# Kernel tuning notes

Hardware: AMD Instinct MI355X
Metric: run time of the kernel (lower is better)

Reference implementation:

```python
import jax, jax.numpy as jnp
import numpy as np

V = 4          # view_num
B = 2048       # batch_size
D = 512        # feature dim
N = V * B
TEMP = 0.5     # temperature
EPS = 1e-8     # torch CosineSimilarity eps


def _neg_idx():
    # Row with residue p (position within its view block) masks out columns c
    # with c % B == p (the positive/self positions), exactly matching
    # mask_positive_samples: fill_diagonal_(0) on every BxB block.
    cols = np.arange(N)
    return np.stack([cols[cols % B != p] for p in range(B)])  # [B, N-V]

_NEG_IDX = jnp.asarray(_neg_idx())


def setup_inputs() -> dict:
    key = jax.random.key(0)
    x = jax.random.normal(key, (V, B, D), dtype=jnp.float32)
    return {"x": x}


def reference(x):
    # torch.cat(input, dim=0) -> [N, D]
    xf = x.reshape(N, D)
    # Cosine similarity via normalize + matmul (same math as broadcasted
    # CosineSimilarity(dim=2), expressed efficiently).
    norm = jnp.maximum(jnp.linalg.norm(xf, axis=1, keepdims=True), EPS)
    xn = xf / norm
    sim = (xn @ xn.T) / TEMP                                  # [N, N]

    # Negatives per anchor row: gather masked columns (same column order as
    # torch boolean-mask indexing, which is row-major ascending).
    sim_v = sim.reshape(V, B, N)
    negs = jnp.take_along_axis(sim_v, _NEG_IDX[None], axis=2)  # [V, B, N-V]
    lse_neg = jax.nn.logsumexp(negs, axis=2)                   # [V, B]

    # pos[i, j, b] = sim block-diagonal between views i and j
    pos = jnp.diagonal(sim.reshape(V, B, V, B), axis1=1, axis2=3)  # [V, V, B]

    # CrossEntropy with label 0 on logits = [pos_ij, negatives_i]:
    #   loss_b = logsumexp([pos, negs]) - pos = logaddexp(pos, lse_neg) - pos
    lse = jnp.logaddexp(pos, lse_neg[:, None, :])              # [V, V, B]
    per_pair = (lse - pos).sum(axis=2) / B                     # [V, V]

    off_diag = 1.0 - jnp.eye(V, dtype=per_pair.dtype)          # skip j == i
    return jnp.sum(per_pair * off_diag)
```

## Files before the change

kernel.cpp:

```cpp
#include <hip/hip_runtime.h>
#include <hip/hip_fp8.h>

#define NV 4
#define NB 2048
#define ND 512
#define NN 8192

typedef int int8v __attribute__((ext_vector_type(8)));
typedef int int4v __attribute__((ext_vector_type(4)));
typedef float floatx4 __attribute__((ext_vector_type(4)));
#define SCALE1 0x7F7F7F7Fu

__global__ __launch_bounds__(256) void normalize_k(const float* __restrict__ x,
                                                   unsigned char* __restrict__ xn,
                                                   float* __restrict__ sumexp,
                                                   float* __restrict__ out) {
  if (threadIdx.x < 4) sumexp[blockIdx.x * 4 + threadIdx.x] = 0.0f;
  if (blockIdx.x == 0 && threadIdx.x == 0) out[0] = 0.0f;

  const int row = blockIdx.x * 4 + (threadIdx.x >> 6);
  const int l = threadIdx.x & 63;
  const float4* xr = (const float4*)(x + (size_t)row * ND);
  float4 v0 = xr[l * 2 + 0];
  float4 v1 = xr[l * 2 + 1];
  float ss = v0.x * v0.x + v0.y * v0.y + v0.z * v0.z + v0.w * v0.w +
             v1.x * v1.x + v1.y * v1.y + v1.z * v1.z + v1.w * v1.w;
#pragma unroll
  for (int off = 32; off > 0; off >>= 1) ss += __shfl_xor(ss, off, 64);
  const float inv = 1.0f / fmaxf(sqrtf(ss), 1e-8f);
  union { unsigned char b[8]; uint2 u; } pk;
  pk.b[0] = __hip_fp8_e4m3(v0.x * inv).__x;
  pk.b[1] = __hip_fp8_e4m3(v0.y * inv).__x;
  pk.b[2] = __hip_fp8_e4m3(v0.z * inv).__x;
  pk.b[3] = __hip_fp8_e4m3(v0.w * inv).__x;
  pk.b[4] = __hip_fp8_e4m3(v1.x * inv).__x;
  pk.b[5] = __hip_fp8_e4m3(v1.y * inv).__x;
  pk.b[6] = __hip_fp8_e4m3(v1.z * inv).__x;
  pk.b[7] = __hip_fp8_e4m3(v1.w * inv).__x;
  *(uint2*)(xn + (size_t)row * ND + l * 8) = pk.u;
}

__global__ __launch_bounds__(256) void sim_k(const unsigned char* __restrict__ xn,
                                             float* __restrict__ sumexp,
                                             float* __restrict__ pos) {
  __shared__ unsigned char As[128 * 128];
  __shared__ unsigned char Bs[128 * 128];
  const int tid = threadIdx.x;
  const int l = tid & 63;
  const int m = l & 15, q = l >> 4, s = l & 7;
  const int wr = (tid >> 6) >> 1, wc = (tid >> 6) & 1;

  const int bid = blockIdx.x;
  int rt = (int)((129.0f - sqrtf(16641.0f - 8.0f * (float)bid)) * 0.5f);
  rt = rt < 0 ? 0 : (rt > 63 ? 63 : rt);
  while (rt > 0 && (rt * 64 - rt * (rt - 1) / 2) > bid) --rt;
  while (rt < 63 && ((rt + 1) * 64 - (rt + 1) * rt / 2) <= bid) ++rt;
  const int ct = rt + (bid - (rt * 64 - rt * (rt - 1) / 2));
  const bool diag = (rt == ct);

  floatx4 acc[4][4] = {};

  const unsigned char* gA = xn + (size_t)rt * 128 * ND;
  const unsigned char* gB = xn + (size_t)ct * 128 * ND;

  const int crow = tid >> 3;
  const int coff = (tid & 7) * 16;
  const int lsw = ((tid & 7) ^ ((tid >> 3) & 7)) * 16;

  const int fo0 = ((2 * q + 0) ^ s) * 16;
  const int fo1 = ((2 * q + 1) ^ s) * 16;

  int4v pA[4], pB[4];
#pragma unroll
  for (int i = 0; i < 4; ++i) {
    const size_t go = (size_t)(i * 32 + crow) * ND + coff;
    pA[i] = *(const int4v*)(gA + go);
    pB[i] = *(const int4v*)(gB + go);
  }

#pragma unroll 1
  for (int kt = 0; kt < 4; ++kt) {
#pragma unroll
    for (int i = 0; i < 4; ++i) {
      const int la = (i * 32 + crow) * 128 + lsw;
      *(int4v*)(As + la) = pA[i];
      *(int4v*)(Bs + la) = pB[i];
    }
    __syncthreads();
    if (kt < 3) {
      const int kb = (kt + 1) * 128;
#pragma unroll
      for (int i = 0; i < 4; ++i) {
        const size_t go = (size_t)(i * 32 + crow) * ND + kb + coff;
        pA[i] = *(const int4v*)(gA + go);
        pB[i] = *(const int4v*)(gB + go);
      }
    }
    int8v af0, af1, af2, af3, bf0, bf1, bf2, bf3;
    {
      const unsigned char* pa0 = As + (wr * 64 + 0 * 16 + m) * 128;
      const unsigned char* pa1 = As + (wr * 64 + 1 * 16 + m) * 128;
      const unsigned char* pa2 = As + (wr * 64 + 2 * 16 + m) * 128;
      const unsigned char* pa3 = As + (wr * 64 + 3 * 16 + m) * 128;
      const unsigned char* pb0 = Bs + (wc * 64 + 0 * 16 + m) * 128;
      const unsigned char* pb1 = Bs + (wc * 64 + 1 * 16 + m) * 128;
      const unsigned char* pb2 = Bs + (wc * 64 + 2 * 16 + m) * 128;
      const unsigned char* pb3 = Bs + (wc * 64 + 3 * 16 + m) * 128;
      af0 = __builtin_shufflevector(*(const int4v*)(pa0 + fo0),
                                    *(const int4v*)(pa0 + fo1), 0,1,2,3,4,5,6,7);
      af1 = __builtin_shufflevector(*(const int4v*)(pa1 + fo0),
                                    *(const int4v*)(pa1 + fo1), 0,1,2,3,4,5,6,7);
      af2 = __builtin_shufflevector(*(const int4v*)(pa2 + fo0),
                                    *(const int4v*)(pa2 + fo1), 0,1,2,3,4,5,6,7);
      af3 = __builtin_shufflevector(*(const int4v*)(pa3 + fo0),
                                    *(const int4v*)(pa3 + fo1), 0,1,2,3,4,5,6,7);
      bf0 = __builtin_shufflevector(*(const int4v*)(pb0 + fo0),
                                    *(const int4v*)(pb0 + fo1), 0,1,2,3,4,5,6,7);
      bf1 = __builtin_shufflevector(*(const int4v*)(pb1 + fo0),
                                    *(const int4v*)(pb1 + fo1), 0,1,2,3,4,5,6,7);
      bf2 = __builtin_shufflevector(*(const int4v*)(pb2 + fo0),
                                    *(const int4v*)(pb2 + fo1), 0,1,2,3,4,5,6,7);
      bf3 = __builtin_shufflevector(*(const int4v*)(pb3 + fo0),
                                    *(const int4v*)(pb3 + fo1), 0,1,2,3,4,5,6,7);
    }
#define MFMA_ROW(mt, afv)                                                     \
  acc[mt][0] = __builtin_amdgcn_mfma_scale_f32_16x16x128_f8f6f4(              \
      afv, bf0, acc[mt][0], 0, 0, 0, SCALE1, 0, SCALE1);                      \
  acc[mt][1] = __builtin_amdgcn_mfma_scale_f32_16x16x128_f8f6f4(              \
      afv, bf1, acc[mt][1], 0, 0, 0, SCALE1, 0, SCALE1);                      \
  acc[mt][2] = __builtin_amdgcn_mfma_scale_f32_16x16x128_f8f6f4(              \
      afv, bf2, acc[mt][2], 0, 0, 0, SCALE1, 0, SCALE1);                      \
  acc[mt][3] = __builtin_amdgcn_mfma_scale_f32_16x16x128_f8f6f4(              \
      afv, bf3, acc[mt][3], 0, 0, 0, SCALE1, 0, SCALE1)
    MFMA_ROW(0, af0);
    MFMA_ROW(1, af1);
    MFMA_ROW(2, af2);
    MFMA_ROW(3, af3);
#undef MFMA_ROW
    __syncthreads();
  }

  const int r0 = rt * 128 + wr * 64;
  const int c0 = ct * 128 + wc * 64;
  float cs[4] = {0.f, 0.f, 0.f, 0.f};
#pragma unroll
  for (int mt = 0; mt < 4; ++mt) {
    float rs[4] = {0.f, 0.f, 0.f, 0.f};
#pragma unroll
    for (int nt = 0; nt < 4; ++nt) {
      const int c = c0 + nt * 16 + m;
#pragma unroll
      for (int reg = 0; reg < 4; ++reg) {
        const int r = r0 + mt * 16 + q * 4 + reg;
        const float sv = acc[mt][nt][reg] * 2.0f;
        if (((c - r) & (NB - 1)) == 0) {
          pos[r * NV + (c >> 11)] = sv;
          if (!diag) pos[c * NV + (r >> 11)] = sv;
        } else {
          const float e = __expf(sv);
          rs[reg] += e;
          cs[nt] += e;
        }
      }
    }
#pragma unroll
    for (int off = 1; off < 16; off <<= 1) {
#pragma unroll
      for (int reg = 0; reg < 4; ++reg) rs[reg] += __shfl_xor(rs[reg], off, 64);
    }
    if (m < 4) atomicAdd(&sumexp[r0 + mt * 16 + q * 4 + m], rs[m]);
  }
  if (!diag) {
#pragma unroll
    for (int nt = 0; nt < 4; ++nt) {
      cs[nt] += __shfl_xor(cs[nt], 16, 64);
      cs[nt] += __shfl_xor(cs[nt], 32, 64);
    }
    if (q == 0) {
#pragma unroll
      for (int nt = 0; nt < 4; ++nt)
        atomicAdd(&sumexp[c0 + nt * 16 + m], cs[nt]);
    }
  }
}

__global__ __launch_bounds__(256) void finalize_k(
    const float* __restrict__ sumexp, const float* __restrict__ pos,
    float* __restrict__ out) {
  const int r = blockIdx.x * 256 + threadIdx.x;
  const float se = sumexp[r];
  const int i = r >> 11;
  float local = 0.0f;
#pragma unroll
  for (int j = 0; j < NV; ++j) {
    if (j == i) continue;
    const float p = pos[r * NV + j];
    local += logf(__expf(p) + se) - p;
  }
  local *= (1.0f / NB);
#pragma unroll
  for (int off = 32; off > 0; off >>= 1) local += __shfl_xor(local, off, 64);
  if ((threadIdx.x & 63) == 0) atomicAdd(out, local);
}

extern "C" void kernel_launch(void* const* d_in, const int* in_sizes, int n_in,
                              void* d_out, int out_size, void* d_ws,
                              size_t ws_size, hipStream_t stream) {
  const float* x = (const float*)d_in[0];
  float* out = (float*)d_out;
  char* ws = (char*)d_ws;
  unsigned char* xn = (unsigned char*)ws;
  float* sumexp = (float*)(ws + (size_t)NN * ND);
  float* pos = (float*)(ws + (size_t)NN * ND + NN * 4);

  normalize_k<<<NN / 4, 256, 0, stream>>>(x, xn, sumexp, out);
  sim_k<<<64 * 65 / 2, 256, 0, stream>>>(xn, sumexp, pos);
  finalize_k<<<NN / 256, 256, 0, stream>>>(sumexp, pos, out);
}
```

Baseline: 110.0 us.

## Enlarge similarity tiles to 256x256 with 8 waves and double-buffered LDS

The fused similarity kernel moves from 128x128 tiles with 4 waves to 256x256 tiles with 512 threads, 8 waves of 128x64 each. The upper-triangle tile mapping is recomputed for a 32x32 tile grid. Shared memory is double-buffered so the trailing barrier in the K loop can be dropped, and MFMA issue is wrapped in s_setprio. The goal is more operand reuse per LDS byte, less global traffic and fewer barriers. In exchange it uses 128KB of LDS per block, so likely only one block fits per CU, and launches only 528 blocks, which risks poor CU balance and a tail.

After: 113.2 us. 3.0% more time.

```diff
diff --git a/kernel.cpp b/kernel.cpp
--- a/kernel.cpp
+++ b/kernel.cpp
@@ -40,28 +40,29 @@
   *(uint2*)(xn + (size_t)row * ND + l * 8) = pk.u;
 }
 
-__global__ __launch_bounds__(256) void sim_k(const unsigned char* __restrict__ xn,
-                                             float* __restrict__ sumexp,
-                                             float* __restrict__ pos) {
-  __shared__ unsigned char As[128 * 128];
-  __shared__ unsigned char Bs[128 * 128];
+__global__ __launch_bounds__(512, 2) void sim_k(const unsigned char* __restrict__ xn,
+                                                float* __restrict__ sumexp,
+                                                float* __restrict__ pos) {
+  __shared__ unsigned char As[2 * 256 * 128];
+  __shared__ unsigned char Bs[2 * 256 * 128];
   const int tid = threadIdx.x;
   const int l = tid & 63;
   const int m = l & 15, q = l >> 4, s = l & 7;
-  const int wr = (tid >> 6) >> 1, wc = (tid >> 6) & 1;
+  const int wid = tid >> 6;
+  const int wr = wid >> 2, wc = wid & 3;
 
   const int bid = blockIdx.x;
-  int rt = (int)((129.0f - sqrtf(16641.0f - 8.0f * (float)bid)) * 0.5f);
-  rt = rt < 0 ? 0 : (rt > 63 ? 63 : rt);
-  while (rt > 0 && (rt * 64 - rt * (rt - 1) / 2) > bid) --rt;
-  while (rt < 63 && ((rt + 1) * 64 - (rt + 1) * rt / 2) <= bid) ++rt;
-  const int ct = rt + (bid - (rt * 64 - rt * (rt - 1) / 2));
+  int rt = (int)((65.0f - sqrtf(4225.0f - 8.0f * (float)bid)) * 0.5f);
+  rt = rt < 0 ? 0 : (rt > 31 ? 31 : rt);
+  while (rt > 0 && (rt * (65 - rt) / 2) > bid) --rt;
+  while (rt < 31 && ((rt + 1) * (64 - rt) / 2) <= bid) ++rt;
+  const int ct = rt + (bid - rt * (65 - rt) / 2);
   const bool diag = (rt == ct);
 
-  floatx4 acc[4][4] = {};
-
-  const unsigned char* gA = xn + (size_t)rt * 128 * ND;
-  const unsigned char* gB = xn + (size_t)ct * 128 * ND;
+  floatx4 acc[8][4] = {};
+
+  const unsigned char* gA = xn + (size_t)rt * 256 * ND;
+  const unsigned char* gB = xn + (size_t)ct * 256 * ND;
 
   const int crow = tid >> 3;
   const int coff = (tid & 7) * 16;
@@ -73,47 +74,37 @@
   int4v pA[4], pB[4];
 #pragma unroll
   for (int i = 0; i < 4; ++i) {
-    const size_t go = (size_t)(i * 32 + crow) * ND + coff;
+    const size_t go = (size_t)(i * 64 + crow) * ND + coff;
     pA[i] = *(const int4v*)(gA + go);
     pB[i] = *(const int4v*)(gB + go);
   }
 
 #pragma unroll 1
   for (int kt = 0; kt < 4; ++kt) {
+    unsigned char* Ab = As + (kt & 1) * (256 * 128);
+    unsigned char* Bb = Bs + (kt & 1) * (256 * 128);
 #pragma unroll
     for (int i = 0; i < 4; ++i) {
-      const int la = (i * 32 + crow) * 128 + lsw;
-      *(int4v*)(As + la) = pA[i];
-      *(int4v*)(Bs + la) = pB[i];
+      const int la = (i * 64 + crow) * 128 + lsw;
+      *(int4v*)(Ab + la) = pA[i];
+      *(int4v*)(Bb + la) = pB[i];
     }
     __syncthreads();
     if (kt < 3) {
       const int kb = (kt + 1) * 128;
 #pragma unroll
       for (int i = 0; i < 4; ++i) {
-        const size_t go = (size_t)(i * 32 + crow) * ND + kb + coff;
+        const size_t go = (size_t)(i * 64 + crow) * ND + kb + coff;
         pA[i] = *(const int4v*)(gA + go);
         pB[i] = *(const int4v*)(gB + go);
       }
     }
-    int8v af0, af1, af2, af3, bf0, bf1, bf2, bf3;
+    int8v bf0, bf1, bf2, bf3;
     {
-      const unsigned char* pa0 = As + (wr * 64 + 0 * 16 + m) * 128;
-      const unsigned char* pa1 = As + (wr * 64 + 1 * 16 + m) * 128;
-      const unsigned char* pa2 = As + (wr * 64 + 2 * 16 + m) * 128;
-      const unsigned char* pa3 = As + (wr * 64 + 3 * 16 + m) * 128;
-      const unsigned char* pb0 = Bs + (wc * 64 + 0 * 16 + m) * 128;
-      const unsigned char* pb1 = Bs + (wc * 64 + 1 * 16 + m) * 128;
-      const unsigned char* pb2 = Bs + (wc * 64 + 2 * 16 + m) * 128;
-      const unsigned char* pb3 = Bs + (wc * 64 + 3 * 16 + m) * 128;
-      af0 = __builtin_shufflevector(*(const int4v*)(pa0 + fo0),
-                                    *(const int4v*)(pa0 + fo1), 0,1,2,3,4,5,6,7);
-      af1 = __builtin_shufflevector(*(const int4v*)(pa1 + fo0),
-                                    *(const int4v*)(pa1 + fo1), 0,1,2,3,4,5,6,7);
-      af2 = __builtin_shufflevector(*(const int4v*)(pa2 + fo0),
-                                    *(const int4v*)(pa2 + fo1), 0,1,2,3,4,5,6,7);
-      af3 = __builtin_shufflevector(*(const int4v*)(pa3 + fo0),
-                                    *(const int4v*)(pa3 + fo1), 0,1,2,3,4,5,6,7);
+      const unsigned char* pb0 = Bb + (wc * 64 + 0 * 16 + m) * 128;
+      const unsigned char* pb1 = Bb + (wc * 64 + 1 * 16 + m) * 128;
+      const unsigned char* pb2 = Bb + (wc * 64 + 2 * 16 + m) * 128;
+      const unsigned char* pb3 = Bb + (wc * 64 + 3 * 16 + m) * 128;
       bf0 = __builtin_shufflevector(*(const int4v*)(pb0 + fo0),
                                     *(const int4v*)(pb0 + fo1), 0,1,2,3,4,5,6,7);
       bf1 = __builtin_shufflevector(*(const int4v*)(pb1 + fo0),
@@ -123,28 +114,30 @@
       bf3 = __builtin_shufflevector(*(const int4v*)(pb3 + fo0),
                                     *(const int4v*)(pb3 + fo1), 0,1,2,3,4,5,6,7);
     }
-#define MFMA_ROW(mt, afv)                                                     \
-  acc[mt][0] = __builtin_amdgcn_mfma_scale_f32_16x16x128_f8f6f4(              \
-      afv, bf0, acc[mt][0], 0, 0, 0, SCALE1, 0, SCALE1);                      \
-  acc[mt][1] = __builtin_amdgcn_mfma_scale_f32_16x16x128_f8f6f4(              \
-      afv, bf1, acc[mt][1], 0, 0, 0, SCALE1, 0, SCALE1);                      \
-  acc[mt][2] = __builtin_amdgcn_mfma_scale_f32_16x16x128_f8f6f4(              \
-      afv, bf2, acc[mt][2], 0, 0, 0, SCALE1, 0, SCALE1);                      \
-  acc[mt][3] = __builtin_amdgcn_mfma_scale_f32_16x16x128_f8f6f4(              \
-      afv, bf3, acc[mt][3], 0, 0, 0, SCALE1, 0, SCALE1)
-    MFMA_ROW(0, af0);
-    MFMA_ROW(1, af1);
-    MFMA_ROW(2, af2);
-    MFMA_ROW(3, af3);
-#undef MFMA_ROW
-    __syncthreads();
-  }
-
-  const int r0 = rt * 128 + wr * 64;
-  const int c0 = ct * 128 + wc * 64;
+    __builtin_amdgcn_s_setprio(1);
+#pragma unroll
+    for (int mt = 0; mt < 8; ++mt) {
+      const unsigned char* pa = Ab + (wr * 128 + mt * 16 + m) * 128;
+      const int8v af = __builtin_shufflevector(*(const int4v*)(pa + fo0),
+                                               *(const int4v*)(pa + fo1),
+                                               0,1,2,3,4,5,6,7);
+      acc[mt][0] = __builtin_amdgcn_mfma_scale_f32_16x16x128_f8f6f4(
+          af, bf0, acc[mt][0], 0, 0, 0, SCALE1, 0, SCALE1);
+      acc[mt][1] = __builtin_amdgcn_mfma_scale_f32_16x16x128_f8f6f4(
+          af, bf1, acc[mt][1], 0, 0, 0, SCALE1, 0, SCALE1);
+      acc[mt][2] = __builtin_amdgcn_mfma_scale_f32_16x16x128_f8f6f4(
+          af, bf2, acc[mt][2], 0, 0, 0, SCALE1, 0, SCALE1);
+      acc[mt][3] = __builtin_amdgcn_mfma_scale_f32_16x16x128_f8f6f4(
+          af, bf3, acc[mt][3], 0, 0, 0, SCALE1, 0, SCALE1);
+    }
+    __builtin_amdgcn_s_setprio(0);
+  }
+
+  const int r0 = rt * 256 + wr * 128;
+  const int c0 = ct * 256 + wc * 64;
   float cs[4] = {0.f, 0.f, 0.f, 0.f};
 #pragma unroll
-  for (int mt = 0; mt < 4; ++mt) {
+  for (int mt = 0; mt < 8; ++mt) {
     float rs[4] = {0.f, 0.f, 0.f, 0.f};
 #pragma unroll
     for (int nt = 0; nt < 4; ++nt) {
@@ -214,6 +207,6 @@
   float* pos = (float*)(ws + (size_t)NN * ND + NN * 4);
 
   normalize_k<<<NN / 4, 256, 0, stream>>>(x, xn, sumexp, out);
-  sim_k<<<64 * 65 / 2, 256, 0, stream>>>(xn, sumexp, pos);
+  sim_k<<<32 * 33 / 2, 512, 0, stream>>>(xn, sumexp, pos);
   finalize_k<<<NN / 256, 256, 0, stream>>>(sumexp, pos, out);
 }
```

## Load full-K tiles via direct global-to-LDS loads and swizzle block order

Applied to the files above, without the earlier changes.

The sim kernel now stages the entire 128x512 fp8 A and B tiles into LDS up front with global_load_lds (direct-to-LDS) instructions. This replaces the register-staged, four-step K pipeline that needed a barrier per step. The block index is also remapped in groups of eight to change the tile scheduling order, likely to spread work across XCDs or improve cache locality. LDS per block grows to 128 KB with launch_bounds(256,1), so occupancy drops to one block per CU and there is no overlap between load and compute inside a block.

Result: slower. 131.2 us (+19.3%).

```diff
diff --git a/kernel.cpp b/kernel.cpp
--- a/kernel.cpp
+++ b/kernel.cpp
@@ -40,17 +40,18 @@
   *(uint2*)(xn + (size_t)row * ND + l * 8) = pk.u;
 }
 
-__global__ __launch_bounds__(256) void sim_k(const unsigned char* __restrict__ xn,
-                                             float* __restrict__ sumexp,
-                                             float* __restrict__ pos) {
-  __shared__ unsigned char As[128 * 128];
-  __shared__ unsigned char Bs[128 * 128];
+__global__ __launch_bounds__(256, 1) void sim_k(const unsigned char* __restrict__ xn,
+                                                float* __restrict__ sumexp,
+                                                float* __restrict__ pos) {
+  __shared__ unsigned char As[128 * 512];
+  __shared__ unsigned char Bs[128 * 512];
   const int tid = threadIdx.x;
   const int l = tid & 63;
   const int m = l & 15, q = l >> 4, s = l & 7;
-  const int wr = (tid >> 6) >> 1, wc = (tid >> 6) & 1;
-
-  const int bid = blockIdx.x;
+  const int w = tid >> 6;
+  const int wr = w >> 1, wc = w & 1;
+
+  const int bid = (blockIdx.x & 7) * 260 + (blockIdx.x >> 3);
   int rt = (int)((129.0f - sqrtf(16641.0f - 8.0f * (float)bid)) * 0.5f);
   rt = rt < 0 ? 0 : (rt > 63 ? 63 : rt);
   while (rt > 0 && (rt * 64 - rt * (rt - 1) / 2) > bid) --rt;
@@ -58,86 +59,73 @@
   const int ct = rt + (bid - (rt * 64 - rt * (rt - 1) / 2));
   const bool diag = (rt == ct);
 
-  floatx4 acc[4][4] = {};
-
   const unsigned char* gA = xn + (size_t)rt * 128 * ND;
   const unsigned char* gB = xn + (size_t)ct * 128 * ND;
 
-  const int crow = tid >> 3;
-  const int coff = (tid & 7) * 16;
-  const int lsw = ((tid & 7) ^ ((tid >> 3) & 7)) * 16;
+#define GLL16(gp, lp)                                                        \
+  __builtin_amdgcn_global_load_lds(                                          \
+      (const __attribute__((address_space(1))) void*)(gp),                   \
+      (__attribute__((address_space(3))) void*)(lp), 16, 0, 0)
+
+  {
+    int swz[4];
+#pragma unroll
+    for (int j = 0; j < 4; ++j)
+      swz[j] = ((l & 31) ^ ((2 * j + (l >> 5)) & 7)) * 16;
+    const size_t lrow = (size_t)(l >> 5) * 512;
+    if (w < 2) {
+      const int g0 = w * 32;
+#pragma unroll
+      for (int i = 0; i < 32; ++i)
+        GLL16(gA + lrow + (size_t)(g0 + i) * 1024 + swz[i & 3],
+              As + (g0 + i) * 1024);
+    } else {
+      const int g0 = (w - 2) * 32;
+#pragma unroll
+      for (int i = 0; i < 32; ++i)
+        GLL16(gB + lrow + (size_t)(g0 + i) * 1024 + swz[i & 3],
+              Bs + (g0 + i) * 1024);
+    }
+  }
+  __syncthreads();
 
   const int fo0 = ((2 * q + 0) ^ s) * 16;
   const int fo1 = ((2 * q + 1) ^ s) * 16;
-
-  int4v pA[4], pB[4];
-#pragma unroll
-  for (int i = 0; i < 4; ++i) {
-    const size_t go = (size_t)(i * 32 + crow) * ND + coff;
-    pA[i] = *(const int4v*)(gA + go);
-    pB[i] = *(const int4v*)(gB + go);
-  }
-
-#pragma unroll 1
+  floatx4 acc[4][4] = {};
+
+#define LDFRAG(dst, base, row, kt)                                           \
+  do {                                                                       \
+    const unsigned char* p_ = (base) + (size_t)(row) * 512 + (kt) * 128;     \
+    dst = __builtin_shufflevector(*(const int4v*)(p_ + fo0),                 \
+                                  *(const int4v*)(p_ + fo1),                 \
+                                  0, 1, 2, 3, 4, 5, 6, 7);                   \
+  } while (0)
+
+#pragma unroll
   for (int kt = 0; kt < 4; ++kt) {
-#pragma unroll
-    for (int i = 0; i < 4; ++i) {
-      const int la = (i * 32 + crow) * 128 + lsw;
-      *(int4v*)(As + la) = pA[i];
-      *(int4v*)(Bs + la) = pB[i];
-    }
-    __syncthreads();
-    if (kt < 3) {
-      const int kb = (kt + 1) * 128;
-#pragma unroll
-      for (int i = 0; i < 4; ++i) {
-        const size_t go = (size_t)(i * 32 + crow) * ND + kb + coff;
-        pA[i] = *(const int4v*)(gA + go);
-        pB[i] = *(const int4v*)(gB + go);
-      }
-    }
     int8v af0, af1, af2, af3, bf0, bf1, bf2, bf3;
-    {
-      const unsigned char* pa0 = As + (wr * 64 + 0 * 16 + m) * 128;
-      const unsigned char* pa1 = As + (wr * 64 + 1 * 16 + m) * 128;
-      const unsigned char* pa2 = As + (wr * 64 + 2 * 16 + m) * 128;
-      const unsigned char* pa3 = As + (wr * 64 + 3 * 16 + m) * 128;
-      const unsigned char* pb0 = Bs + (wc * 64 + 0 * 16 + m) * 128;
-      const unsigned char* pb1 = Bs + (wc * 64 + 1 * 16 + m) * 128;
-      const unsigned char* pb2 = Bs + (wc * 64 + 2 * 16 + m) * 128;
-      const unsigned char* pb3 = Bs + (wc * 64 + 3 * 16 + m) * 128;
-      af0 = __builtin_shufflevector(*(const int4v*)(pa0 + fo0),
-                                    *(const int4v*)(pa0 + fo1), 0,1,2,3,4,5,6,7);
-      af1 = __builtin_shufflevector(*(const int4v*)(pa1 + fo0),
-                                    *(const int4v*)(pa1 + fo1), 0,1,2,3,4,5,6,7);
-      af2 = __builtin_shufflevector(*(const int4v*)(pa2 + fo0),
-                                    *(const int4v*)(pa2 + fo1), 0,1,2,3,4,5,6,7);
-      af3 = __builtin_shufflevector(*(const int4v*)(pa3 + fo0),
-                                    *(const int4v*)(pa3 + fo1), 0,1,2,3,4,5,6,7);
-      bf0 = __builtin_shufflevector(*(const int4v*)(pb0 + fo0),
-                                    *(const int4v*)(pb0 + fo1), 0,1,2,3,4,5,6,7);
-      bf1 = __builtin_shufflevector(*(const int4v*)(pb1 + fo0),
-                                    *(const int4v*)(pb1 + fo1), 0,1,2,3,4,5,6,7);
-      bf2 = __builtin_shufflevector(*(const int4v*)(pb2 + fo0),
-                                    *(const int4v*)(pb2 + fo1), 0,1,2,3,4,5,6,7);
-      bf3 = __builtin_shufflevector(*(const int4v*)(pb3 + fo0),
-                                    *(const int4v*)(pb3 + fo1), 0,1,2,3,4,5,6,7);
-    }
-#define MFMA_ROW(mt, afv)                                                     \
-  acc[mt][0] = __builtin_amdgcn_mfma_scale_f32_16x16x128_f8f6f4(              \
-      afv, bf0, acc[mt][0], 0, 0, 0, SCALE1, 0, SCALE1);                      \
-  acc[mt][1] = __builtin_amdgcn_mfma_scale_f32_16x16x128_f8f6f4(              \
-      afv, bf1, acc[mt][1], 0, 0, 0, SCALE1, 0, SCALE1);                      \
-  acc[mt][2] = __builtin_amdgcn_mfma_scale_f32_16x16x128_f8f6f4(              \
-      afv, bf2, acc[mt][2], 0, 0, 0, SCALE1, 0, SCALE1);                      \
-  acc[mt][3] = __builtin_amdgcn_mfma_scale_f32_16x16x128_f8f6f4(              \
+    LDFRAG(af0, As, wr * 64 + 0 * 16 + m, kt);
+    LDFRAG(af1, As, wr * 64 + 1 * 16 + m, kt);
+    LDFRAG(af2, As, wr * 64 + 2 * 16 + m, kt);
+    LDFRAG(af3, As, wr * 64 + 3 * 16 + m, kt);
+    LDFRAG(bf0, Bs, wc * 64 + 0 * 16 + m, kt);
+    LDFRAG(bf1, Bs, wc * 64 + 1 * 16 + m, kt);
+    LDFRAG(bf2, Bs, wc * 64 + 2 * 16 + m, kt);
+    LDFRAG(bf3, Bs, wc * 64 + 3 * 16 + m, kt);
+#define MFMA_ROW(mt, afv)                                                    \
+  acc[mt][0] = __builtin_amdgcn_mfma_scale_f32_16x16x128_f8f6f4(             \
+      afv, bf0, acc[mt][0], 0, 0, 0, SCALE1, 0, SCALE1);                     \
+  acc[mt][1] = __builtin_amdgcn_mfma_scale_f32_16x16x128_f8f6f4(             \
+      afv, bf1, acc[mt][1], 0, 0, 0, SCALE1, 0, SCALE1);                     \
+  acc[mt][2] = __builtin_amdgcn_mfma_scale_f32_16x16x128_f8f6f4(             \
+      afv, bf2, acc[mt][2], 0, 0, 0, SCALE1, 0, SCALE1);                     \
+  acc[mt][3] = __builtin_amdgcn_mfma_scale_f32_16x16x128_f8f6f4(             \
       afv, bf3, acc[mt][3], 0, 0, 0, SCALE1, 0, SCALE1)
     MFMA_ROW(0, af0);
     MFMA_ROW(1, af1);
     MFMA_ROW(2, af2);
     MFMA_ROW(3, af3);
 #undef MFMA_ROW
-    __syncthreads();
   }
 
   const int r0 = rt * 128 + wr * 64;
```

## Fuse normalize, similarity and finalize into one cooperative persistent kernel

Applied to the files above, without the earlier changes.

Replaces three kernel launches with a single cooperative kernel of 512 persistent blocks. Grid-wide syncs separate the normalize, similarity-tile and finalize phases. Tiles are assigned by striding, with a permuted mapping that spreads work across blocks. This removes launch gaps and inter-kernel drains, at the cost of grid.sync overhead and a fixed 512-block grid, which may under-fill the device. The three-kernel path is kept as a fallback if the cooperative launch fails.

Measured after the change: 221.9 us. 2.02x slower.

```diff
diff --git a/kernel.cpp b/kernel.cpp
--- a/kernel.cpp
+++ b/kernel.cpp
@@ -1,5 +1,8 @@
 #include <hip/hip_runtime.h>
+#include <hip/hip_cooperative_groups.h>
 #include <hip/hip_fp8.h>
+
+namespace cg = cooperative_groups;
 
 #define NV 4
 #define NB 2048
@@ -10,6 +13,212 @@
 typedef int int4v __attribute__((ext_vector_type(4)));
 typedef float floatx4 __attribute__((ext_vector_type(4)));
 #define SCALE1 0x7F7F7F7Fu
+
+
+
+__global__ __launch_bounds__(256) void fused_k(const float* __restrict__ x,
+                                               unsigned char* __restrict__ xn,
+                                               float* __restrict__ sumexp,
+                                               float* __restrict__ pos,
+                                               float* __restrict__ out) {
+  __shared__ unsigned char As[128 * 128];
+  __shared__ unsigned char Bs[128 * 128];
+  cg::grid_group grid = cg::this_grid();
+
+  const int tid = threadIdx.x;
+  const int bid0 = blockIdx.x;
+
+  {
+    const int gid = bid0 * 256 + tid;
+    if (gid < NN) sumexp[gid] = 0.0f;
+    if (gid == 0) out[0] = 0.0f;
+
+    const int wg = bid0 * 4 + (tid >> 6);
+    const int l = tid & 63;
+#pragma unroll 1
+    for (int i = 0; i < 4; ++i) {
+      const int row = wg + 2048 * i;
+      const float4* xr = (const float4*)(x + (size_t)row * ND);
+      float4 v0 = xr[l * 2 + 0];
+      float4 v1 = xr[l * 2 + 1];
+      float ss = v0.x * v0.x + v0.y * v0.y + v0.z * v0.z + v0.w * v0.w +
+                 v1.x * v1.x + v1.y * v1.y + v1.z * v1.z + v1.w * v1.w;
+#pragma unroll
+      for (int off = 32; off > 0; off >>= 1) ss += __shfl_xor(ss, off, 64);
+      const float inv = 1.0f / fmaxf(sqrtf(ss), 1e-8f);
+      union { unsigned char b[8]; uint2 u; } pk;
+      pk.b[0] = __hip_fp8_e4m3(v0.x * inv).__x;
+      pk.b[1] = __hip_fp8_e4m3(v0.y * inv).__x;
+      pk.b[2] = __hip_fp8_e4m3(v0.z * inv).__x;
+      pk.b[3] = __hip_fp8_e4m3(v0.w * inv).__x;
+      pk.b[4] = __hip_fp8_e4m3(v1.x * inv).__x;
+      pk.b[5] = __hip_fp8_e4m3(v1.y * inv).__x;
+      pk.b[6] = __hip_fp8_e4m3(v1.z * inv).__x;
+      pk.b[7] = __hip_fp8_e4m3(v1.w * inv).__x;
+      *(uint2*)(xn + (size_t)row * ND + l * 8) = pk.u;
+    }
+  }
+
+  grid.sync();
+
+  {
+    const int l = tid & 63;
+    const int m = l & 15, q = l >> 4, s = l & 7;
+    const int wr = (tid >> 6) >> 1, wc = (tid >> 6) & 1;
+    const int crow = tid >> 3;
+    const int coff = (tid & 7) * 16;
+    const int lsw = ((tid & 7) ^ ((tid >> 3) & 7)) * 16;
+    const int fo0 = ((2 * q + 0) ^ s) * 16;
+    const int fo1 = ((2 * q + 1) ^ s) * 16;
+
+#pragma unroll 1
+    for (int tt = bid0; tt < 2080; tt += 512) {
+      const int bid = (tt & 7) * 260 + (tt >> 3);
+      int rt = (int)((129.0f - sqrtf(16641.0f - 8.0f * (float)bid)) * 0.5f);
+      rt = rt < 0 ? 0 : (rt > 63 ? 63 : rt);
+      while (rt > 0 && (rt * 64 - rt * (rt - 1) / 2) > bid) --rt;
+      while (rt < 63 && ((rt + 1) * 64 - (rt + 1) * rt / 2) <= bid) ++rt;
+      const int ct = rt + (bid - (rt * 64 - rt * (rt - 1) / 2));
+      const bool diag = (rt == ct);
+
+      floatx4 acc[4][4] = {};
+      const unsigned char* gA = xn + (size_t)rt * 128 * ND;
+      const unsigned char* gB = xn + (size_t)ct * 128 * ND;
+
+      int4v pA[4], pB[4];
+#pragma unroll
+      for (int i = 0; i < 4; ++i) {
+        const size_t go = (size_t)(i * 32 + crow) * ND + coff;
+        pA[i] = *(const int4v*)(gA + go);
+        pB[i] = *(const int4v*)(gB + go);
+      }
+
+#pragma unroll 1
+      for (int kt = 0; kt < 4; ++kt) {
+#pragma unroll
+        for (int i = 0; i < 4; ++i) {
+          const int la = (i * 32 + crow) * 128 + lsw;
+          *(int4v*)(As + la) = pA[i];
+          *(int4v*)(Bs + la) = pB[i];
+        }
+        __syncthreads();
+        if (kt < 3) {
+          const int kb = (kt + 1) * 128;
+#pragma unroll
+          for (int i = 0; i < 4; ++i) {
+            const size_t go = (size_t)(i * 32 + crow) * ND + kb + coff;
+            pA[i] = *(const int4v*)(gA + go);
+            pB[i] = *(const int4v*)(gB + go);
+          }
+        }
+        int8v af0, af1, af2, af3, bf0, bf1, bf2, bf3;
+        {
+          const unsigned char* pa0 = As + (wr * 64 + 0 * 16 + m) * 128;
+          const unsigned char* pa1 = As + (wr * 64 + 1 * 16 + m) * 128;
+          const unsigned char* pa2 = As + (wr * 64 + 2 * 16 + m) * 128;
+          const unsigned char* pa3 = As + (wr * 64 + 3 * 16 + m) * 128;
+          const unsigned char* pb0 = Bs + (wc * 64 + 0 * 16 + m) * 128;
+          const unsigned char* pb1 = Bs + (wc * 64 + 1 * 16 + m) * 128;
+          const unsigned char* pb2 = Bs + (wc * 64 + 2 * 16 + m) * 128;
+          const unsigned char* pb3 = Bs + (wc * 64 + 3 * 16 + m) * 128;
+          af0 = __builtin_shufflevector(*(const int4v*)(pa0 + fo0),
+                                        *(const int4v*)(pa0 + fo1), 0,1,2,3,4,5,6,7);
+          af1 = __builtin_shufflevector(*(const int4v*)(pa1 + fo0),
+                                        *(const int4v*)(pa1 + fo1), 0,1,2,3,4,5,6,7);
+          af2 = __builtin_shufflevector(*(const int4v*)(pa2 + fo0),
+                                        *(const int4v*)(pa2 + fo1), 0,1,2,3,4,5,6,7);
+          af3 = __builtin_shufflevector(*(const int4v*)(pa3 + fo0),
+                                        *(const int4v*)(pa3 + fo1), 0,1,2,3,4,5,6,7);
+          bf0 = __builtin_shufflevector(*(const int4v*)(pb0 + fo0),
+                                        *(const int4v*)(pb0 + fo1), 0,1,2,3,4,5,6,7);
+          bf1 = __builtin_shufflevector(*(const int4v*)(pb1 + fo0),
+                                        *(const int4v*)(pb1 + fo1), 0,1,2,3,4,5,6,7);
+          bf2 = __builtin_shufflevector(*(const int4v*)(pb2 + fo0),
+                                        *(const int4v*)(pb2 + fo1), 0,1,2,3,4,5,6,7);
+          bf3 = __builtin_shufflevector(*(const int4v*)(pb3 + fo0),
+                                        *(const int4v*)(pb3 + fo1), 0,1,2,3,4,5,6,7);
+        }
+#define MFMA_ROW(mt, afv)                                                     \
+  acc[mt][0] = __builtin_amdgcn_mfma_scale_f32_16x16x128_f8f6f4(              \
+      afv, bf0, acc[mt][0], 0, 0, 0, SCALE1, 0, SCALE1);                      \
+  acc[mt][1] = __builtin_amdgcn_mfma_scale_f32_16x16x128_f8f6f4(              \
+      afv, bf1, acc[mt][1], 0, 0, 0, SCALE1, 0, SCALE1);                      \
+  acc[mt][2] = __builtin_amdgcn_mfma_scale_f32_16x16x128_f8f6f4(              \
+      afv, bf2, acc[mt][2], 0, 0, 0, SCALE1, 0, SCALE1);                      \
+  acc[mt][3] = __builtin_amdgcn_mfma_scale_f32_16x16x128_f8f6f4(              \
+      afv, bf3, acc[mt][3], 0, 0, 0, SCALE1, 0, SCALE1)
+        MFMA_ROW(0, af0);
+        MFMA_ROW(1, af1);
+        MFMA_ROW(2, af2);
+        MFMA_ROW(3, af3);
+#undef MFMA_ROW
+        __syncthreads();
+      }
+
+      const int r0 = rt * 128 + wr * 64;
+      const int c0 = ct * 128 + wc * 64;
+      float cs[4] = {0.f, 0.f, 0.f, 0.f};
+#pragma unroll
+      for (int mt = 0; mt < 4; ++mt) {
+        float rs[4] = {0.f, 0.f, 0.f, 0.f};
+#pragma unroll
+        for (int nt = 0; nt < 4; ++nt) {
+          const int c = c0 + nt * 16 + m;
+#pragma unroll
+          for (int reg = 0; reg < 4; ++reg) {
+            const int r = r0 + mt * 16 + q * 4 + reg;
+            const float sv = acc[mt][nt][reg] * 2.0f;
+            if (((c - r) & (NB - 1)) == 0) {
+              pos[r * NV + (c >> 11)] = sv;
+              if (!diag) pos[c * NV + (r >> 11)] = sv;
+            } else {
+              const float e = __expf(sv);
+              rs[reg] += e;
+              cs[nt] += e;
+            }
+          }
+        }
+#pragma unroll
+        for (int off = 1; off < 16; off <<= 1) {
+#pragma unroll
+          for (int reg = 0; reg < 4; ++reg) rs[reg] += __shfl_xor(rs[reg], off, 64);
+        }
+        if (m < 4) atomicAdd(&sumexp[r0 + mt * 16 + q * 4 + m], rs[m]);
+      }
+      if (!diag) {
+#pragma unroll
+        for (int nt = 0; nt < 4; ++nt) {
+          cs[nt] += __shfl_xor(cs[nt], 16, 64);
+          cs[nt] += __shfl_xor(cs[nt], 32, 64);
+        }
+        if (q == 0) {
+#pragma unroll
+          for (int nt = 0; nt < 4; ++nt)
+            atomicAdd(&sumexp[c0 + nt * 16 + m], cs[nt]);
+        }
+      }
+    }
+  }
+
+  grid.sync();
+
+  if (bid0 < NN / 256) {
+    const int r = bid0 * 256 + tid;
+    const float se = sumexp[r];
+    const int i = r >> 11;
+    float local = 0.0f;
+#pragma unroll
+    for (int j = 0; j < NV; ++j) {
+      if (j == i) continue;
+      const float p = pos[r * NV + j];
+      local += logf(__expf(p) + se) - p;
+    }
+    local *= (1.0f / NB);
+#pragma unroll
+    for (int off = 32; off > 0; off >>= 1) local += __shfl_xor(local, off, 64);
+    if ((tid & 63) == 0) atomicAdd(out, local);
+  }
+}
 
 __global__ __launch_bounds__(256) void normalize_k(const float* __restrict__ x,
                                                    unsigned char* __restrict__ xn,
@@ -17,7 +226,6 @@
                                                    float* __restrict__ out) {
   if (threadIdx.x < 4) sumexp[blockIdx.x * 4 + threadIdx.x] = 0.0f;
   if (blockIdx.x == 0 && threadIdx.x == 0) out[0] = 0.0f;
-
   const int row = blockIdx.x * 4 + (threadIdx.x >> 6);
   const int l = threadIdx.x & 63;
   const float4* xr = (const float4*)(x + (size_t)row * ND);
@@ -40,6 +248,25 @@
   *(uint2*)(xn + (size_t)row * ND + l * 8) = pk.u;
 }
 
+__global__ __launch_bounds__(256) void finalize_k(
+    const float* __restrict__ sumexp, const float* __restrict__ pos,
+    float* __restrict__ out) {
+  const int r = blockIdx.x * 256 + threadIdx.x;
+  const float se = sumexp[r];
+  const int i = r >> 11;
+  float local = 0.0f;
+#pragma unroll
+  for (int j = 0; j < NV; ++j) {
+    if (j == i) continue;
+    const float p = pos[r * NV + j];
+    local += logf(__expf(p) + se) - p;
+  }
+  local *= (1.0f / NB);
+#pragma unroll
+  for (int off = 32; off > 0; off >>= 1) local += __shfl_xor(local, off, 64);
+  if ((threadIdx.x & 63) == 0) atomicAdd(out, local);
+}
+
 __global__ __launch_bounds__(256) void sim_k(const unsigned char* __restrict__ xn,
                                              float* __restrict__ sumexp,
                                              float* __restrict__ pos) {
@@ -49,7 +276,6 @@
   const int l = tid & 63;
   const int m = l & 15, q = l >> 4, s = l & 7;
   const int wr = (tid >> 6) >> 1, wc = (tid >> 6) & 1;
-
   const int bid = blockIdx.x;
   int rt = (int)((129.0f - sqrtf(16641.0f - 8.0f * (float)bid)) * 0.5f);
   rt = rt < 0 ? 0 : (rt > 63 ? 63 : rt);
@@ -57,19 +283,14 @@
   while (rt < 63 && ((rt + 1) * 64 - (rt + 1) * rt / 2) <= bid) ++rt;
   const int ct = rt + (bid - (rt * 64 - rt * (rt - 1) / 2));
   const bool diag = (rt == ct);
-
   floatx4 acc[4][4] = {};
-
   const unsigned char* gA = xn + (size_t)rt * 128 * ND;
   const unsigned char* gB = xn + (size_t)ct * 128 * ND;
-
   const int crow = tid >> 3;
   const int coff = (tid & 7) * 16;
   const int lsw = ((tid & 7) ^ ((tid >> 3) & 7)) * 16;
-
   const int fo0 = ((2 * q + 0) ^ s) * 16;
   const int fo1 = ((2 * q + 1) ^ s) * 16;
-
   int4v pA[4], pB[4];
 #pragma unroll
   for (int i = 0; i < 4; ++i) {
@@ -77,7 +298,6 @@
     pA[i] = *(const int4v*)(gA + go);
     pB[i] = *(const int4v*)(gB + go);
   }
-
 #pragma unroll 1
   for (int kt = 0; kt < 4; ++kt) {
 #pragma unroll
@@ -139,7 +359,6 @@
 #undef MFMA_ROW
     __syncthreads();
   }
-
   const int r0 = rt * 128 + wr * 64;
   const int c0 = ct * 128 + wc * 64;
   float cs[4] = {0.f, 0.f, 0.f, 0.f};
@@ -184,25 +403,6 @@
   }
 }
 
-__global__ __launch_bounds__(256) void finalize_k(
-    const float* __restrict__ sumexp, const float* __restrict__ pos,
-    float* __restrict__ out) {
-  const int r = blockIdx.x * 256 + threadIdx.x;
-  const float se = sumexp[r];
-  const int i = r >> 11;
-  float local = 0.0f;
-#pragma unroll
-  for (int j = 0; j < NV; ++j) {
-    if (j == i) continue;
-    const float p = pos[r * NV + j];
-    local += logf(__expf(p) + se) - p;
-  }
-  local *= (1.0f / NB);
-#pragma unroll
-  for (int off = 32; off > 0; off >>= 1) local += __shfl_xor(local, off, 64);
-  if ((threadIdx.x & 63) == 0) atomicAdd(out, local);
-}
-
 extern "C" void kernel_launch(void* const* d_in, const int* in_sizes, int n_in,
                               void* d_out, int out_size, void* d_ws,
                               size_t ws_size, hipStream_t stream) {
@@ -213,7 +413,13 @@
   float* sumexp = (float*)(ws + (size_t)NN * ND);
   float* pos = (float*)(ws + (size_t)NN * ND + NN * 4);
 
-  normalize_k<<<NN / 4, 256, 0, stream>>>(x, xn, sumexp, out);
-  sim_k<<<64 * 65 / 2, 256, 0, stream>>>(xn, sumexp, pos);
-  finalize_k<<<NN / 256, 256, 0, stream>>>(sumexp, pos, out);
+  void* args[] = {(void*)&x, (void*)&xn, (void*)&sumexp, (void*)&pos,
+                  (void*)&out};
+  hipError_t err = hipLaunchCooperativeKernel(
+      (const void*)(const void*)fused_k, dim3(512), dim3(256), args, 0, stream);
+  if (err != hipSuccess) {
+    normalize_k<<<NN / 4, 256, 0, stream>>>(x, xn, sumexp, out);
+    sim_k<<<64 * 65 / 2, 256, 0, stream>>>(xn, sumexp, pos);
+    finalize_k<<<NN / 256, 256, 0, stream>>>(sumexp, pos, out);
+  }
 }
```
